# Optimization experiments

Hardware: AMD Instinct MI355X
Metric: run time of the kernel (lower is better)

The kernel has to match this reference:

```python
import jax, jax.numpy as jnp
import numpy as np

SCALE = 4


def _dist_mats():
    # Replicates matrix_generation() with scale=4 (numpy constants).
    s = SCALE
    x = np.array([-2.0, -1.0, 1.0, 2.0], np.float32)  # arange(-2,3) with the 0 removed
    base = np.broadcast_to(x[None, :], (s, s)).copy()  # varies along width
    dm = np.stack([base, base.T])[None]                # [1,2,4,4]
    xr = np.broadcast_to(np.arange(1, s + 1, dtype=np.float32)[None, :], (s, s)).copy()
    xc = xr.T
    dm1 = dm.copy(); dm1[:, 0] = s - xr + 1
    dm2 = dm.copy(); dm2[:, 0] = xr
    dm3 = dm.copy(); dm3[:, 1] = s - xc + 1
    dm4 = dm.copy(); dm4[:, 1] = xc
    # NOTE: forward() reuses dm1..dm4 for the 4 diagonal directions (as in the
    # original code, which indexes self.distance_matrix1..4 for matrices 5..8).
    return dm, dm1, dm2, dm3, dm4


def _mlp(x, w0, w1, w2, w3):
    # 1x1-conv stack 66->32->16->8->1, no bias, LeakyReLU(0.01) between.
    h = jax.nn.leaky_relu(jnp.einsum('bchw,oc->bohw', x, w0))
    h = jax.nn.leaky_relu(jnp.einsum('bchw,oc->bohw', h, w1))
    h = jax.nn.leaky_relu(jnp.einsum('bchw,oc->bohw', h, w2))
    return jnp.einsum('bchw,oc->bohw', h, w3)


def setup_inputs() -> dict:
    key = jax.random.key(0)
    ks = jax.random.split(key, 8)
    B, C, H, W = 2, 32, 256, 512
    lr_feature = jax.random.normal(ks[0], (B, C, H // SCALE, W // SCALE), jnp.float32)
    hr_feature = jax.random.normal(ks[1], (B, C, H, W), jnp.float32)
    lr_feature_r = jax.random.normal(ks[2], (B, C, H // SCALE, W // SCALE), jnp.float32)
    hr_feature_r = jax.random.normal(ks[3], (B, C, H, W), jnp.float32)
    # kaiming_normal_(mode='fan_out') for 1x1 conv: std = sqrt(2 / out_ch)
    def kaiming(k, shape):
        return jax.random.normal(k, shape, jnp.float32) * np.sqrt(2.0 / shape[0]).astype(np.float32)
    w0 = kaiming(ks[4], (32, 66))
    w1 = kaiming(ks[5], (16, 32))
    w2 = kaiming(ks[6], (8, 16))
    w3 = kaiming(ks[7], (1, 8))
    return {'lr_feature': lr_feature, 'hr_feature': hr_feature,
            'lr_feature_r': lr_feature_r, 'hr_feature_r': hr_feature_r,
            'w0': w0, 'w1': w1, 'w2': w2, 'w3': w3}


def reference(lr_feature, hr_feature, lr_feature_r, hr_feature_r, w0, w1, w2, w3):
    s = SCALE
    B, _, H, W = hr_feature.shape
    dm, dm1, dm2, dm3, dm4 = _dist_mats()
    tile = lambda d: jnp.tile(jnp.asarray(d), (B, 1, H // s, W // s))  # [B,2,H,W]
    D, D1, D2, D3, D4 = tile(dm), tile(dm1), tile(dm2), tile(dm3), tile(dm4)
    # nearest-neighbor upsample of lr feature by scale in both spatial dims
    lr = jnp.repeat(jnp.repeat(lr_feature, s, axis=3), s, axis=2)
    hr = hr_feature
    pad1 = jnp.full((B, 1, H, s), -100.0, hr.dtype)  # width padding
    pad2 = jnp.full((B, 1, s, W), -100.0, hr.dtype)  # height padding
    cat = lambda *xs: jnp.concatenate(xs, axis=1)
    m = lambda x: _mlp(x, w0, w1, w2, w3)

    w_c = m(cat(lr, hr, D))
    w_l = jnp.concatenate([pad1, m(cat(lr[:, :, :, :-s], hr[:, :, :, s:], D1[:, :, :, :-s]))], -1)
    w_r = jnp.concatenate([m(cat(lr[:, :, :, s:], hr[:, :, :, :-s], D2[:, :, :, s:])), pad1], -1)
    w_t = jnp.concatenate([pad2, m(cat(lr[:, :, :-s, :], hr[:, :, s:, :], D3[:, :, :-s, :]))], -2)
    w_b = jnp.concatenate([m(cat(lr[:, :, s:, :], hr[:, :, :-s, :], D4[:, :, s:, :])), pad2], -2)
    w_lt = jnp.concatenate([pad2, jnp.concatenate(
        [pad1[:, :, s:, :], m(cat(lr[:, :, :-s, :-s], hr[:, :, s:, s:], D1[:, :, :-s, :-s]))], -1)], -2)
    w_rt = jnp.concatenate([pad2, jnp.concatenate(
        [m(cat(lr[:, :, :-s, s:], hr[:, :, s:, :-s], D2[:, :, :-s, s:])), pad1[:, :, s:, :]], -1)], -2)
    w_lb = jnp.concatenate([jnp.concatenate(
        [pad1[:, :, s:, :], m(cat(lr[:, :, s:, :-s], hr[:, :, :-s, s:], D3[:, :, s:, :-s]))], -1), pad2], -2)
    w_rb = jnp.concatenate([jnp.concatenate(
        [m(cat(lr[:, :, s:, s:], hr[:, :, :-s, :-s], D4[:, :, s:, s:])), pad1[:, :, :-s, :]], -1), pad2], -2)

    weight_all = jnp.concatenate([w_c, w_l, w_r, w_t, w_b, w_lt, w_rt, w_lb, w_rb], axis=1)
    # Original returns the 9 channel slices of softmax(weight_all, dim=1);
    # we return the full normalized [B,9,H,W] tensor (slice i == output i).
    return jax.nn.softmax(weight_all, axis=1)
```

## Files before the change

### kernel.cpp

```cpp
#include <hip/hip_runtime.h>
#include <math.h>

#define SC 4
#define BB 2
#define CC 32
#define HH 256
#define WW 512
#define CH (HH / SC)
#define CW (WW / SC)

using f16x8 = __attribute__((ext_vector_type(8))) _Float16;
using f32x4 = __attribute__((ext_vector_type(4))) float;
using f32x2 = __attribute__((ext_vector_type(2))) float;

constexpr int K_dh[9] = {0, 0, 0, -1, 1, -1, -1, 1, 1};
constexpr int K_dw[9] = {0, -1, 1, 0, 0, -1, 1, -1, 1};
constexpr int K_s0[9] = {0, 1, 2, 0, 0, 1, 2, 0, 0};
constexpr int K_s1[9] = {0, 0, 0, 1, 2, 0, 0, 1, 2};

template <int CTRL>
__device__ __forceinline__ float dpp_add(float v) {
    union { float f; int i; } u, r;
    u.f = v;
    r.i = __builtin_amdgcn_update_dpp(0, u.i, CTRL, 0xF, 0xF, true);
    return v + r.f;
}

__device__ __forceinline__ float sum16(float v) {
    v = dpp_add<0xB1>(v);
    v = dpp_add<0x4E>(v);
    v = dpp_add<0x141>(v);
    v = dpp_add<0x140>(v);
    return v;
}

__global__ __launch_bounds__(256) void alr_prepass(const float* __restrict__ lr,
                                                   const float* __restrict__ w0,
                                                   float* __restrict__ alr) {
    const int idx = blockIdx.x * 256 + threadIdx.x;
    if (idx >= BB * CH * CW) return;
    const int b = idx / (CH * CW);
    const int cell = idx - b * (CH * CW);
    const float* lp = lr + (size_t)b * CC * CH * CW + cell;
    float lv[32];
#pragma unroll
    for (int c = 0; c < 32; c++) lv[c] = lp[(size_t)c * (CH * CW)];
    float acc[32];
#pragma unroll
    for (int o = 0; o < 32; o++) {
        float a = 0.f;
#pragma unroll
        for (int c = 0; c < 32; c++) a = fmaf(lv[c], w0[o * 66 + c], a);
        acc[o] = a;
    }
    float4* op = (float4*)(alr + (size_t)idx * 32);
#pragma unroll
    for (int j = 0; j < 8; j++)
        op[j] = make_float4(acc[4 * j], acc[4 * j + 1], acc[4 * j + 2], acc[4 * j + 3]);
}

template <bool USE_WS>
__global__ __launch_bounds__(256, 4) void ercm_mfma(const float* __restrict__ hr,
                                                    const float* __restrict__ lr,
                                                    const float* __restrict__ alr,
                                                    const float* __restrict__ w0,
                                                    const float* __restrict__ w1,
                                                    const float* __restrict__ w2,
                                                    const float* __restrict__ w3,
                                                    float* __restrict__ out) {
    __shared__ _Float16 s_alr[54 * 40];
    __shared__ _Float16 s_ahr[4][16 * 40];
    __shared__ _Float16 s_d2[4][16 * 40];

    const int tid = threadIdx.x;
    const int lane = tid & 63;
    const int ty = tid >> 6;
    const int m16 = lane & 15;
    const int q = lane >> 4;
    const int bx = blockIdx.x;
    const int by = blockIdx.y;
    const int b = blockIdx.z;
    const int h = by * 4 + ty;
    const int wp0 = bx * 64;
    const size_t HW = (size_t)HH * WW;

    const int cy0 = by, cx0 = bx * 16;
    if (USE_WS) {
        for (int i = tid; i < 54 * 32; i += 256) {
            const int c = i & 31, cell = i >> 5;
            const int row = cell / 18, col = cell - row * 18;
            const int gcy = cy0 - 1 + row, gcx = cx0 - 1 + col;
            float v = 0.f;
            if ((unsigned)gcy < (unsigned)CH && (unsigned)gcx < (unsigned)CW)
                v = alr[(((size_t)b * CH + gcy) * CW + gcx) * 32 + c];
            s_alr[cell * 40 + c] = (_Float16)v;
        }
    } else {
        for (int i = tid; i < 54 * 32; i += 256) {
            const int o = i & 31, cell = i >> 5;
            const int row = cell / 18, col = cell - row * 18;
            const int gcy = cy0 - 1 + row, gcx = cx0 - 1 + col;
            float a = 0.f;
            if ((unsigned)gcy < (unsigned)CH && (unsigned)gcx < (unsigned)CW) {
                const float* lp = lr + (size_t)b * CC * CH * CW + (size_t)gcy * CW + gcx;
#pragma unroll
                for (int c = 0; c < 32; c++) a = fmaf(lp[(size_t)c * (CH * CW)], w0[o * 66 + c], a);
            }
            s_alr[cell * 40 + o] = (_Float16)a;
        }
    }

    f16x8 w1B, w0hB0, w0hB1, w2B;
    {
        const float* p1 = w1 + m16 * 32 + q * 8;
        const float* p00 = w0 + m16 * 66 + 32 + q * 8;
        const float* p01 = w0 + (m16 + 16) * 66 + 32 + q * 8;
        const bool w2ok = (m16 < 8) && (q < 2);
#pragma unroll
        for (int j = 0; j < 8; j++) {
            w1B[j] = (_Float16)p1[j];
            w0hB0[j] = (_Float16)p00[j];
            w0hB1[j] = (_Float16)p01[j];
            w2B[j] = (_Float16)(w2ok ? w2[m16 * 16 + q * 8 + j] : 0.f);
        }
    }
    f32x2 w0d0v[4], w0d1v[4];
#pragma unroll
    for (int jp = 0; jp < 4; jp++) {
        w0d0v[jp] = f32x2{w0[(q * 8 + 2 * jp) * 66 + 64], w0[(q * 8 + 2 * jp + 1) * 66 + 64]};
        w0d1v[jp] = f32x2{w0[(q * 8 + 2 * jp) * 66 + 65], w0[(q * 8 + 2 * jp + 1) * 66 + 65]};
    }
    const float w3v = (m16 < 8) ? w3[m16] : 0.f;

    const int xm = m16 & 3;
    const float xv = (float)(xm < 2 ? xm - 2 : xm - 1);
    const float x1 = (float)(4 - xm), x2 = (float)(xm + 1);
    const int ym = h & 3;
    const float yv = (float)(ym < 2 ? ym - 2 : ym - 1);
    const float y1 = (float)(4 - ym), y2 = (float)(ym + 1);

    _Float16* sa = s_ahr[ty];
    _Float16* sd = s_d2[ty];
#pragma unroll
    for (int r = 0; r < 4; r++) sd[(q * 4 + r) * 40 + 16 + m16] = (_Float16)0.f;

    __syncthreads();

    const float* hp = hr + (size_t)b * CC * HW + (size_t)h * WW + wp0;

#pragma unroll 1
    for (int t = 0; t < 4; t++) {
        f16x8 a;
#pragma unroll
        for (int j = 0; j < 8; j++) a[j] = (_Float16)hp[(size_t)(q * 8 + j) * HW + t * 16 + m16];
        f32x4 acc0 = {0.f, 0.f, 0.f, 0.f}, acc1 = {0.f, 0.f, 0.f, 0.f};
        acc0 = __builtin_amdgcn_mfma_f32_16x16x32_f16(a, w0hB0, acc0, 0, 0, 0);
        acc1 = __builtin_amdgcn_mfma_f32_16x16x32_f16(a, w0hB1, acc1, 0, 0, 0);
#pragma unroll
        for (int r = 0; r < 4; r++) {
            sa[(q * 4 + r) * 40 + m16] = (_Float16)acc0[r];
            sa[(q * 4 + r) * 40 + 16 + m16] = (_Float16)acc1[r];
        }
        const f16x8 ahv = *(const f16x8*)&sa[m16 * 40 + q * 8];
        f32x2 ah2[4];
#pragma unroll
        for (int jp = 0; jp < 4; jp++)
            ah2[jp] = f32x2{(float)ahv[2 * jp], (float)ahv[2 * jp + 1]};

        const _Float16* alp = &s_alr[((t * 16 + m16) >> 2) * 40 + q * 8];
        const int wown = wp0 + t * 16 + q * 4 + xm;

        float l[9];
#pragma unroll
        for (int d = 0; d < 9; d++) {
            const int dh = K_dh[d], dw = K_dw[d];
            const float d0 = (K_s0[d] == 0) ? xv : ((K_s0[d] == 1) ? x1 : x2);
            const float d1 = (K_s1[d] == 0) ? yv : ((K_s1[d] == 1) ? y1 : y2);
            const f32x2 d0v = {d0, d0}, d1v = {d1, d1};

            const f16x8 alv = *(const f16x8*)(alp + ((1 + dh) * 18 + (1 + dw)) * 40);
            f16x8 a1;
#pragma unroll
            for (int jp = 0; jp < 4; jp++) {
                f32x2 v = ah2[jp] + f32x2{(float)alv[2 * jp], (float)alv[2 * jp + 1]};
                v = __builtin_elementwise_fma(w0d0v[jp], d0v, v);
                v = __builtin_elementwise_fma(w0d1v[jp], d1v, v);
                v = __builtin_elementwise_max(v, v * 0.01f);
                a1[2 * jp] = (_Float16)v[0];
                a1[2 * jp + 1] = (_Float16)v[1];
            }
            f32x4 acc2 = {0.f, 0.f, 0.f, 0.f};
            acc2 = __builtin_amdgcn_mfma_f32_16x16x32_f16(a1, w1B, acc2, 0, 0, 0);
#pragma unroll
            for (int r = 0; r < 4; r++) {
                const float v = fmaxf(acc2[r], 0.01f * acc2[r]);
                sd[(q * 4 + r) * 40 + m16] = (_Float16)v;
            }
            const f16x8 a3 = *(const f16x8*)&sd[m16 * 40 + q * 8];
            f32x4 acc3 = {0.f, 0.f, 0.f, 0.f};
            acc3 = __builtin_amdgcn_mfma_f32_16x16x32_f16(a3, w2B, acc3, 0, 0, 0);

            float sr[4];
#pragma unroll
            for (int r = 0; r < 4; r++)
                sr[r] = sum16(w3v * fmaxf(acc3[r], 0.01f * acc3[r]));
            float lv = sr[0];
            lv = (xm == 1) ? sr[1] : lv;
            lv = (xm == 2) ? sr[2] : lv;
            lv = (xm == 3) ? sr[3] : lv;
            const bool ok = ((unsigned)(h + 4 * dh) < (unsigned)HH) &&
                            ((unsigned)(wown + 4 * dw) < (unsigned)WW);
            l[d] = ok ? lv : -100.0f;
        }

        float mx = l[0];
#pragma unroll
        for (int d = 1; d < 9; d++) mx = fmaxf(mx, l[d]);
        float s = 0.f;
#pragma unroll
        for (int d = 0; d < 9; d++) {
            l[d] = __expf(l[d] - mx);
            s += l[d];
        }
        const float inv = __builtin_amdgcn_rcpf(s);
        if (m16 < 4) {
            float* op = out + (size_t)b * 9 * HW + (size_t)h * WW + (wp0 + t * 16 + q * 4 + m16);
#pragma unroll
            for (int d = 0; d < 9; d++) op[(size_t)d * HW] = l[d] * inv;
        }
    }
}

extern "C" void kernel_launch(void* const* d_in, const int* in_sizes, int n_in,
                              void* d_out, int out_size, void* d_ws, size_t ws_size,
                              hipStream_t stream) {
    const float* lr = (const float*)d_in[0];
    const float* hr = (const float*)d_in[1];
    const float* w0 = (const float*)d_in[4];
    const float* w1 = (const float*)d_in[5];
    const float* w2 = (const float*)d_in[6];
    const float* w3 = (const float*)d_in[7];
    float* out = (float*)d_out;

    const size_t alr_bytes = (size_t)BB * CH * CW * 32 * sizeof(float);
    dim3 grid(WW / 64, HH / 4, BB);

    if (ws_size >= alr_bytes) {
        float* alr = (float*)d_ws;
        alr_prepass<<<(BB * CH * CW + 255) / 256, 256, 0, stream>>>(lr, w0, alr);
        ercm_mfma<true><<<grid, 256, 0, stream>>>(hr, lr, alr, w0, w1, w2, w3, out);
    } else {
        ercm_mfma<false><<<grid, 256, 0, stream>>>(hr, lr, nullptr, w0, w1, w2, w3, out);
    }
}
```

Before: 153.9 us.

## Transpose MFMA operands, replace LDS round-trips with bpermute and permlane reductions

Restructures the per-thread inner loop. All four 16-pixel tiles are processed together: their hr projections are staged in a larger LDS buffer, and the loop order becomes direction-outer, tile-inner so the distance-term FMAs are hoisted out of the tile loop. The MFMA operands are swapped so that outputs are laid out per column. The layer-2 to layer-3 handoff now uses ds_bpermute in place of an LDS store/load, and the final 8→1 reduction uses permlane16/32 swaps instead of DPP adds. The occupancy hint drops from 4 to 3 blocks per CU, since unrolling all tiles needs more registers; this trades occupancy for instruction-level parallelism.

```diff
diff --git a/kernel.cpp b/kernel.cpp
--- a/kernel.cpp
+++ b/kernel.cpp
@@ -18,20 +18,20 @@
 constexpr int K_s0[9] = {0, 1, 2, 0, 0, 1, 2, 0, 0};
 constexpr int K_s1[9] = {0, 0, 0, 1, 2, 0, 0, 1, 2};
 
-template <int CTRL>
-__device__ __forceinline__ float dpp_add(float v) {
-    union { float f; int i; } u, r;
-    u.f = v;
-    r.i = __builtin_amdgcn_update_dpp(0, u.i, CTRL, 0xF, 0xF, true);
-    return v + r.f;
-}
-
-__device__ __forceinline__ float sum16(float v) {
-    v = dpp_add<0xB1>(v);
-    v = dpp_add<0x4E>(v);
-    v = dpp_add<0x141>(v);
-    v = dpp_add<0x140>(v);
-    return v;
+__device__ __forceinline__ int pack2h(float a, float b) {
+    union { _Float16 h[2]; int i; } u;
+    u.h[0] = (_Float16)a;
+    u.h[1] = (_Float16)b;
+    return u.i;
+}
+
+__device__ __forceinline__ float xsum64(float part) {
+    float a = part, b = part;
+    asm("v_permlane16_swap_b32 %0, %1" : "+v"(a), "+v"(b));
+    float s2 = a + b;
+    a = s2; b = s2;
+    asm("v_permlane32_swap_b32 %0, %1" : "+v"(a), "+v"(b));
+    return a + b;
 }
 
 __global__ __launch_bounds__(256) void alr_prepass(const float* __restrict__ lr,
@@ -60,7 +60,7 @@
 }
 
 template <bool USE_WS>
-__global__ __launch_bounds__(256, 4) void ercm_mfma(const float* __restrict__ hr,
+__global__ __launch_bounds__(256, 3) void ercm_mfma(const float* __restrict__ hr,
                                                     const float* __restrict__ lr,
                                                     const float* __restrict__ alr,
                                                     const float* __restrict__ w0,
@@ -69,8 +69,7 @@
                                                     const float* __restrict__ w3,
                                                     float* __restrict__ out) {
     __shared__ _Float16 s_alr[54 * 40];
-    __shared__ _Float16 s_ahr[4][16 * 40];
-    __shared__ _Float16 s_d2[4][16 * 40];
+    __shared__ _Float16 s_ahr[4][64 * 40];
 
     const int tid = threadIdx.x;
     const int lane = tid & 63;
@@ -130,7 +129,9 @@
         w0d0v[jp] = f32x2{w0[(q * 8 + 2 * jp) * 66 + 64], w0[(q * 8 + 2 * jp + 1) * 66 + 64]};
         w0d1v[jp] = f32x2{w0[(q * 8 + 2 * jp) * 66 + 65], w0[(q * 8 + 2 * jp + 1) * 66 + 65]};
     }
-    const float w3v = (m16 < 8) ? w3[m16] : 0.f;
+    float w3c[4];
+#pragma unroll
+    for (int r = 0; r < 4; r++) w3c[r] = (q < 2) ? w3[q * 4 + r] : 0.f;
 
     const int xm = m16 & 3;
     const float xv = (float)(xm < 2 ? xm - 2 : xm - 1);
@@ -139,94 +140,115 @@
     const float yv = (float)(ym < 2 ? ym - 2 : ym - 1);
     const float y1 = (float)(4 - ym), y2 = (float)(ym + 1);
 
+    const int A0 = ((m16 + 32 * q) & 63) << 2;
+    const int A1 = ((m16 + 32 * q + 16) & 63) << 2;
+
     _Float16* sa = s_ahr[ty];
-    _Float16* sd = s_d2[ty];
-#pragma unroll
-    for (int r = 0; r < 4; r++) sd[(q * 4 + r) * 40 + 16 + m16] = (_Float16)0.f;
 
     __syncthreads();
 
     const float* hp = hr + (size_t)b * CC * HW + (size_t)h * WW + wp0;
 
-#pragma unroll 1
-    for (int t = 0; t < 4; t++) {
+#pragma unroll
+    for (int T = 0; T < 4; T++) {
         f16x8 a;
 #pragma unroll
-        for (int j = 0; j < 8; j++) a[j] = (_Float16)hp[(size_t)(q * 8 + j) * HW + t * 16 + m16];
-        f32x4 acc0 = {0.f, 0.f, 0.f, 0.f}, acc1 = {0.f, 0.f, 0.f, 0.f};
-        acc0 = __builtin_amdgcn_mfma_f32_16x16x32_f16(a, w0hB0, acc0, 0, 0, 0);
-        acc1 = __builtin_amdgcn_mfma_f32_16x16x32_f16(a, w0hB1, acc1, 0, 0, 0);
+        for (int j = 0; j < 8; j++)
+            a[j] = (_Float16)hp[(size_t)(q * 8 + j) * HW + T * 16 + m16];
+        f32x4 p0 = {0.f, 0.f, 0.f, 0.f}, p1 = {0.f, 0.f, 0.f, 0.f};
+        p0 = __builtin_amdgcn_mfma_f32_16x16x32_f16(a, w0hB0, p0, 0, 0, 0);
+        p1 = __builtin_amdgcn_mfma_f32_16x16x32_f16(a, w0hB1, p1, 0, 0, 0);
 #pragma unroll
         for (int r = 0; r < 4; r++) {
-            sa[(q * 4 + r) * 40 + m16] = (_Float16)acc0[r];
-            sa[(q * 4 + r) * 40 + 16 + m16] = (_Float16)acc1[r];
-        }
-        const f16x8 ahv = *(const f16x8*)&sa[m16 * 40 + q * 8];
-        f32x2 ah2[4];
+            const int row = T * 16 + q * 4 + r;
+            sa[row * 40 + m16] = (_Float16)p0[r];
+            sa[row * 40 + 16 + m16] = (_Float16)p1[r];
+        }
+    }
+    f32x2 ah[4][4];
+#pragma unroll
+    for (int T = 0; T < 4; T++) {
+        const f16x8 ahv = *(const f16x8*)&sa[(T * 16 + m16) * 40 + q * 8];
 #pragma unroll
         for (int jp = 0; jp < 4; jp++)
-            ah2[jp] = f32x2{(float)ahv[2 * jp], (float)ahv[2 * jp + 1]};
-
-        const _Float16* alp = &s_alr[((t * 16 + m16) >> 2) * 40 + q * 8];
-        const int wown = wp0 + t * 16 + q * 4 + xm;
-
-        float l[9];
-#pragma unroll
-        for (int d = 0; d < 9; d++) {
-            const int dh = K_dh[d], dw = K_dw[d];
-            const float d0 = (K_s0[d] == 0) ? xv : ((K_s0[d] == 1) ? x1 : x2);
-            const float d1 = (K_s1[d] == 0) ? yv : ((K_s1[d] == 1) ? y1 : y2);
-            const f32x2 d0v = {d0, d0}, d1v = {d1, d1};
-
-            const f16x8 alv = *(const f16x8*)(alp + ((1 + dh) * 18 + (1 + dw)) * 40);
+            ah[T][jp] = f32x2{(float)ahv[2 * jp], (float)ahv[2 * jp + 1]};
+    }
+
+    float l[4][9];
+#pragma unroll
+    for (int d = 0; d < 9; d++) {
+        const int dh = K_dh[d], dw = K_dw[d];
+        const float d0 = (K_s0[d] == 0) ? xv : ((K_s0[d] == 1) ? x1 : x2);
+        const float d1 = (K_s1[d] == 0) ? yv : ((K_s1[d] == 1) ? y1 : y2);
+        const f32x2 d0v = {d0, d0}, d1v = {d1, d1};
+        const int off = ((1 + dh) * 18 + (1 + dw)) * 40;
+        const bool okh = (unsigned)(h + 4 * dh) < (unsigned)HH;
+
+        f32x2 dd[4];
+#pragma unroll
+        for (int jp = 0; jp < 4; jp++)
+            dd[jp] = __builtin_elementwise_fma(w0d0v[jp], d0v, w0d1v[jp] * d1v);
+
+#pragma unroll
+        for (int T = 0; T < 4; T++) {
+            const f16x8 alv =
+                *(const f16x8*)&s_alr[(T * 4 + (m16 >> 2)) * 40 + q * 8 + off];
             f16x8 a1;
 #pragma unroll
             for (int jp = 0; jp < 4; jp++) {
-                f32x2 v = ah2[jp] + f32x2{(float)alv[2 * jp], (float)alv[2 * jp + 1]};
-                v = __builtin_elementwise_fma(w0d0v[jp], d0v, v);
-                v = __builtin_elementwise_fma(w0d1v[jp], d1v, v);
+                f32x2 v = ah[T][jp] + f32x2{(float)alv[2 * jp], (float)alv[2 * jp + 1]};
+                v = v + dd[jp];
                 v = __builtin_elementwise_max(v, v * 0.01f);
                 a1[2 * jp] = (_Float16)v[0];
                 a1[2 * jp + 1] = (_Float16)v[1];
             }
-            f32x4 acc2 = {0.f, 0.f, 0.f, 0.f};
-            acc2 = __builtin_amdgcn_mfma_f32_16x16x32_f16(a1, w1B, acc2, 0, 0, 0);
+            f32x4 c2 = {0.f, 0.f, 0.f, 0.f};
+            c2 = __builtin_amdgcn_mfma_f32_16x16x32_f16(w1B, a1, c2, 0, 0, 0);
+
+            f16x8 a3;
+            {
+                float e0 = fmaxf(c2[0], 0.01f * c2[0]), e1 = fmaxf(c2[1], 0.01f * c2[1]);
+                float e2 = fmaxf(c2[2], 0.01f * c2[2]), e3 = fmaxf(c2[3], 0.01f * c2[3]);
+                const int pk0 = pack2h(e0, e1), pk1 = pack2h(e2, e3);
+                union { int i[4]; f16x8 v; } u;
+                u.i[0] = __builtin_amdgcn_ds_bpermute(A0, pk0);
+                u.i[1] = __builtin_amdgcn_ds_bpermute(A0, pk1);
+                u.i[2] = __builtin_amdgcn_ds_bpermute(A1, pk0);
+                u.i[3] = __builtin_amdgcn_ds_bpermute(A1, pk1);
+                a3 = u.v;
+            }
+            f32x4 c3 = {0.f, 0.f, 0.f, 0.f};
+            c3 = __builtin_amdgcn_mfma_f32_16x16x32_f16(w2B, a3, c3, 0, 0, 0);
+
+            float part = 0.f;
 #pragma unroll
             for (int r = 0; r < 4; r++) {
-                const float v = fmaxf(acc2[r], 0.01f * acc2[r]);
-                sd[(q * 4 + r) * 40 + m16] = (_Float16)v;
-            }
-            const f16x8 a3 = *(const f16x8*)&sd[m16 * 40 + q * 8];
-            f32x4 acc3 = {0.f, 0.f, 0.f, 0.f};
-            acc3 = __builtin_amdgcn_mfma_f32_16x16x32_f16(a3, w2B, acc3, 0, 0, 0);
-
-            float sr[4];
-#pragma unroll
-            for (int r = 0; r < 4; r++)
-                sr[r] = sum16(w3v * fmaxf(acc3[r], 0.01f * acc3[r]));
-            float lv = sr[0];
-            lv = (xm == 1) ? sr[1] : lv;
-            lv = (xm == 2) ? sr[2] : lv;
-            lv = (xm == 3) ? sr[3] : lv;
-            const bool ok = ((unsigned)(h + 4 * dh) < (unsigned)HH) &&
-                            ((unsigned)(wown + 4 * dw) < (unsigned)WW);
-            l[d] = ok ? lv : -100.0f;
-        }
-
-        float mx = l[0];
-#pragma unroll
-        for (int d = 1; d < 9; d++) mx = fmaxf(mx, l[d]);
+                const float lv = fmaxf(c3[r], 0.01f * c3[r]);
+                part = fmaf(w3c[r], lv, part);
+            }
+            const float lg = xsum64(part);
+            const int wn = wp0 + T * 16 + m16;
+            const bool ok = okh && ((unsigned)(wn + 4 * dw) < (unsigned)WW);
+            l[T][d] = ok ? lg : -100.0f;
+        }
+    }
+
+#pragma unroll
+    for (int T = 0; T < 4; T++) {
+        float mx = l[T][0];
+#pragma unroll
+        for (int d = 1; d < 9; d++) mx = fmaxf(mx, l[T][d]);
         float s = 0.f;
 #pragma unroll
         for (int d = 0; d < 9; d++) {
-            l[d] = __expf(l[d] - mx);
-            s += l[d];
+            l[T][d] = __expf(l[T][d] - mx);
+            s += l[T][d];
         }
         const float inv = __builtin_amdgcn_rcpf(s);
-        if (m16 < 4) {
-            float* op = out + (size_t)b * 9 * HW + (size_t)h * WW + (wp0 + t * 16 + q * 4 + m16);
-#pragma unroll
-            for (int d = 0; d < 9; d++) op[(size_t)d * HW] = l[d] * inv;
+        if (lane < 16) {
+            float* op = out + (size_t)b * 9 * HW + (size_t)h * WW + (wp0 + T * 16 + m16);
+#pragma unroll
+            for (int d = 0; d < 9; d++) op[(size_t)d * HW] = l[T][d] * inv;
         }
     }
 }
```

New measurement: 153.5 us. Within noise of the previous version (-0.3%).
